# Kernel tuning notes

Measured on AMD Instinct MI355X. Metric: run time of the kernel, lower is better.

The kernel has to match this reference:

```python
import jax, jax.numpy as jnp
import numpy as np

ALPHA = 0.2  # LeakyReLU negative slope

def setup_inputs() -> dict:
    key = jax.random.key(0)
    k1, k2, k3 = jax.random.split(key, 3)
    N, F_in, F_out = 8192, 128, 64
    h = jax.random.normal(k1, (N, F_in), dtype=jnp.float32)
    W = jax.random.normal(k2, (F_in, F_out), dtype=jnp.float32) * 0.1
    a = jax.random.normal(k3, (2 * F_out, 1), dtype=jnp.float32) * 0.1
    return {"h": h, "W": W, "a": a}

def reference(h, W, a):
    # Wh: [N, F_out]
    Wh = h @ W
    F_out = Wh.shape[1]
    # Split 'a' into source/dest halves; e_ij = leakyrelu(a1.Wh_i + a2.Wh_j)
    a1 = a[:F_out, 0]   # [F_out]
    a2 = a[F_out:, 0]   # [F_out]
    e_src = Wh @ a1     # [N]
    e_dst = Wh @ a2     # [N]
    e = e_src[:, None] + e_dst[None, :]          # [N, N]
    e = jnp.where(e > 0, e, ALPHA * e)           # leaky relu
    attention = jax.nn.softmax(e, axis=1)        # dropout omitted (eval mode)
    h_prime = attention @ Wh                     # [N, F_out]
    return jax.nn.elu(h_prime)                   # concat=True path
```

## Files before the change

kernel.cpp:

```cpp
#include <hip/hip_runtime.h>


typedef unsigned long long ull;

constexpr int N_ROWS = 8192;
constexpr int F_IN   = 128;
constexpr int F_OUT  = 64;
#define LRELU_ALPHA 0.2f

constexpr int SBLK = 8;
constexpr int NGRP = N_ROWS / SBLK;

constexpr int WS_WH   = 0;
constexpr int WS_ESRC = WS_WH + N_ROWS * F_OUT;
constexpr int WS_KEYA = WS_ESRC + N_ROWS;
constexpr int WS_KEYB = WS_KEYA + 2 * N_ROWS;
constexpr int WS_GS1T = WS_KEYB + 2 * N_ROWS;
constexpr int WS_GS2T = WS_GS1T + F_OUT * NGRP;
constexpr int WS_GD1  = WS_GS2T + F_OUT * NGRP;
constexpr int WS_GD2  = WS_GD1 + NGRP;
constexpr int WS_P1   = WS_GD2 + NGRP;
constexpr int WS_P2   = WS_P1 + (NGRP + 1) * F_OUT;
constexpr int WS_D1   = WS_P2 + (NGRP + 1) * F_OUT;
constexpr int WS_D2   = WS_D1 + (NGRP + 1);
static_assert((WS_KEYA % 2) == 0 && (WS_KEYB % 2) == 0, "keys 8B-aligned");

__device__ __forceinline__ unsigned mono_enc(float f) {
  unsigned u = __float_as_uint(f);
  return u ^ ((u & 0x80000000u) ? 0xFFFFFFFFu : 0x80000000u);
}
__device__ __forceinline__ float mono_dec(unsigned e) {
  unsigned u = e ^ ((e & 0x80000000u) ? 0x80000000u : 0xFFFFFFFFu);
  return __uint_as_float(u);
}

__global__ __launch_bounds__(256) void k1_wh(const float* __restrict__ h,
                                             const float* __restrict__ W,
                                             const float* __restrict__ a,
                                             float* __restrict__ ws) {
  __shared__ float hlds[16 * F_IN];
  __shared__ float alds[2 * F_OUT];
  const int t = threadIdx.x;
  const int row0 = blockIdx.x * 16;

  const float4* hsrc = (const float4*)(h + (long)row0 * F_IN);
  float4* hd = (float4*)hlds;
  hd[t]       = hsrc[t];
  hd[t + 256] = hsrc[t + 256];
  if (t < 2 * F_OUT) alds[t] = a[t];
  __syncthreads();

  const int wave = t >> 6, lane = t & 63;
  const float* hp = hlds + (wave * 4) * F_IN;
  float acc0 = 0.f, acc1 = 0.f, acc2 = 0.f, acc3 = 0.f;

  #pragma unroll 4
  for (int k4 = 0; k4 < F_IN; k4 += 4) {
    float4 h0 = *(const float4*)(hp + k4);
    float4 h1 = *(const float4*)(hp + F_IN + k4);
    float4 h2 = *(const float4*)(hp + 2 * F_IN + k4);
    float4 h3 = *(const float4*)(hp + 3 * F_IN + k4);
    float w0 = W[(k4 + 0) * F_OUT + lane];
    float w1 = W[(k4 + 1) * F_OUT + lane];
    float w2 = W[(k4 + 2) * F_OUT + lane];
    float w3 = W[(k4 + 3) * F_OUT + lane];
    acc0 = fmaf(h0.x, w0, acc0); acc0 = fmaf(h0.y, w1, acc0);
    acc0 = fmaf(h0.z, w2, acc0); acc0 = fmaf(h0.w, w3, acc0);
    acc1 = fmaf(h1.x, w0, acc1); acc1 = fmaf(h1.y, w1, acc1);
    acc1 = fmaf(h1.z, w2, acc1); acc1 = fmaf(h1.w, w3, acc1);
    acc2 = fmaf(h2.x, w0, acc2); acc2 = fmaf(h2.y, w1, acc2);
    acc2 = fmaf(h2.z, w2, acc2); acc2 = fmaf(h2.w, w3, acc2);
    acc3 = fmaf(h3.x, w0, acc3); acc3 = fmaf(h3.y, w1, acc3);
    acc3 = fmaf(h3.z, w2, acc3); acc3 = fmaf(h3.w, w3, acc3);
  }

  const int grow = row0 + wave * 4;
  float* Wh = ws + WS_WH;
  Wh[(grow + 0) * F_OUT + lane] = acc0;
  Wh[(grow + 1) * F_OUT + lane] = acc1;
  Wh[(grow + 2) * F_OUT + lane] = acc2;
  Wh[(grow + 3) * F_OUT + lane] = acc3;

  const float a1 = alds[lane], a2 = alds[F_OUT + lane];
  float s0 = acc0 * a1, s1 = acc1 * a1, s2 = acc2 * a1, s3 = acc3 * a1;
  float d0 = acc0 * a2, d1 = acc1 * a2, d2 = acc2 * a2, d3 = acc3 * a2;
  #pragma unroll
  for (int off = 32; off; off >>= 1) {
    s0 += __shfl_down(s0, off); s1 += __shfl_down(s1, off);
    s2 += __shfl_down(s2, off); s3 += __shfl_down(s3, off);
    d0 += __shfl_down(d0, off); d1 += __shfl_down(d1, off);
    d2 += __shfl_down(d2, off); d3 += __shfl_down(d3, off);
  }
  if (lane == 0) {
    ws[WS_ESRC + grow + 0] = s0; ws[WS_ESRC + grow + 1] = s1;
    ws[WS_ESRC + grow + 2] = s2; ws[WS_ESRC + grow + 3] = s3;
    ull* keys = (ull*)(ws + WS_KEYA);
    keys[grow + 0] = ((ull)mono_enc(d0) << 32) | (unsigned)(grow + 0);
    keys[grow + 1] = ((ull)mono_enc(d1) << 32) | (unsigned)(grow + 1);
    keys[grow + 2] = ((ull)mono_enc(d2) << 32) | (unsigned)(grow + 2);
    keys[grow + 3] = ((ull)mono_enc(d3) << 32) | (unsigned)(grow + 3);
  }
}

__global__ __launch_bounds__(256) void k2a_local(ull* __restrict__ keys) {
  __shared__ ull lk[256];
  const int t = threadIdx.x;
  const int base = blockIdx.x * 256;
  lk[t] = keys[base + t];
  __syncthreads();
  for (int k = 2; k <= 256; k <<= 1) {
    for (int j = k >> 1; j > 0; j >>= 1) {
      int p = t ^ j;
      if (p > t) {
        ull x = lk[t], y = lk[p];
        bool asc = ((t & k) == 0);
        if ((x > y) == asc) { lk[t] = y; lk[p] = x; }
      }
      __syncthreads();
    }
  }
  keys[base + t] = lk[t];
}

template <int RUN>
__global__ __launch_bounds__(256) void k_merge(const ull* __restrict__ src,
                                               ull* __restrict__ dst) {
  const int g = blockIdx.x * 256 + threadIdx.x;
  const ull key = src[g];
  const int pairbase = g & ~(2 * RUN - 1);
  const int local = g - pairbase;
  const bool inA = local < RUN;
  const ull* other = src + pairbase + (inA ? RUN : 0);
  const int idx = inA ? local : (local - RUN);
  int lo = 0, hi = RUN;
  while (lo < hi) {
    int m = (lo + hi) >> 1;
    if (other[m] < key) lo = m + 1; else hi = m;
  }
  dst[pairbase + idx + lo] = key;
}

__global__ __launch_bounds__(256) void k3a_gs(float* __restrict__ ws) {
  const int t = threadIdx.x, wv = t >> 6, lane = t & 63;
  const int g = blockIdx.x * 4 + wv;
  const ull* K = (const ull*)(ws + WS_KEYB);
  const float* Wh = ws + WS_WH;
  float s1 = 0.f, s2 = 0.f, sd1 = 0.f, sd2 = 0.f;
  #pragma unroll
  for (int o = 0; o < SBLK; ++o) {
    ull key = K[(g << 3) + o];
    float d = mono_dec((unsigned)(key >> 32));
    int j = (int)(key & 0xFFFFFFFFu);
    float e1 = __expf(d), e2 = __expf(LRELU_ALPHA * d);
    float v = Wh[j * F_OUT + lane];
    s1 = fmaf(e1, v, s1); s2 = fmaf(e2, v, s2);
    sd1 += e1; sd2 += e2;
  }
  ws[WS_GS1T + lane * NGRP + g] = s1;
  ws[WS_GS2T + lane * NGRP + g] = s2;
  if (lane == 0) { ws[WS_GD1 + g] = sd1; ws[WS_GD2 + g] = sd2; }
}

__global__ __launch_bounds__(1024) void k3b_scan(float* __restrict__ ws) {
  __shared__ float sm[1024];
  const int t = threadIdx.x;
  const int blk = blockIdx.x;
  const float* src;
  int c = 0;
  if (blk < 64)        { c = blk;      src = ws + WS_GS1T + c * NGRP; }
  else if (blk < 128)  { c = blk - 64; src = ws + WS_GS2T + c * NGRP; }
  else if (blk == 128) { src = ws + WS_GD1; }
  else                 { src = ws + WS_GD2; }

  const float x = src[t];
  sm[t] = x;
  __syncthreads();
  for (int off = 1; off < 1024; off <<= 1) {
    float y = (t >= off) ? sm[t - off] : 0.f;
    __syncthreads();
    sm[t] += y;
    __syncthreads();
  }
  const float incl = sm[t];
  const float excl = incl - x;
  if (blk < 64) {
    ws[WS_P1 + t * F_OUT + c] = excl;
    if (t == NGRP - 1) ws[WS_P1 + NGRP * F_OUT + c] = incl;
  } else if (blk < 128) {
    ws[WS_P2 + t * F_OUT + c] = excl;
    if (t == NGRP - 1) ws[WS_P2 + NGRP * F_OUT + c] = incl;
  } else if (blk == 128) {
    ws[WS_D1 + t] = excl;
    if (t == NGRP - 1) ws[WS_D1 + NGRP] = incl;
  } else {
    ws[WS_D2 + t] = excl;
    if (t == NGRP - 1) ws[WS_D2 + NGRP] = incl;
  }
}

__global__ __launch_bounds__(256) void k4_out(const float* __restrict__ ws,
                                              float* __restrict__ out) {
  const int t = threadIdx.x, wv = t >> 6, lane = t & 63;
  const int i = blockIdx.x * 4 + wv;
  const ull* K = (const ull*)(ws + WS_KEYB);
  const float s = ws[WS_ESRC + i];
  const float ns = (s == 0.0f) ? 0.0f : -s;
  const unsigned Ki = mono_enc(ns);

  unsigned m1 = (unsigned)(K[lane << 7] >> 32);
  ull bal1 = __ballot(m1 <= Ki);
  int tl;
  if (bal1 == 0ull) {
    tl = 0;
  } else {
    int L1 = 63 - __clzll((long long)bal1);
    int base = L1 << 7;
    unsigned m2 = (unsigned)(K[base + (lane << 1)] >> 32);
    ull bal2 = __ballot(m2 <= Ki);
    int L2 = 63 - __clzll((long long)bal2);
    int p = base + (L2 << 1) + 1;
    unsigned m3 = (unsigned)(K[p] >> 32);
    tl = p + ((m3 <= Ki) ? 1 : 0);
  }
  const int b = tl >> 3, rr = tl & 7;

  float p1 = ws[WS_P1 + b * F_OUT + lane];
  float p2 = ws[WS_P2 + b * F_OUT + lane];
  float d1 = ws[WS_D1 + b], d2 = ws[WS_D2 + b];
  const float p1tot = ws[WS_P1 + NGRP * F_OUT + lane];
  const float d1tot = ws[WS_D1 + NGRP];
  const float* Wh = ws + WS_WH;

  for (int o = 0; o < rr; ++o) {
    ull key = K[(b << 3) + o];
    float d = mono_dec((unsigned)(key >> 32));
    int j = (int)(key & 0xFFFFFFFFu);
    float e1 = __expf(d), e2 = __expf(LRELU_ALPHA * d);
    float v = Wh[j * F_OUT + lane];
    p1 = fmaf(e1, v, p1); p2 = fmaf(e2, v, p2);
    d1 += e1; d2 += e2;
  }

  const float es1 = __expf(s), es2 = __expf(LRELU_ALPHA * s);
  const float num = es1 * (p1tot - p1) + es2 * p2;
  const float den = es1 * (d1tot - d1) + es2 * d2;
  const float r = num / den;
  out[i * F_OUT + lane] = (r > 0.f) ? r : (__expf(r) - 1.f);
}

extern "C" void kernel_launch(void* const* d_in, const int* in_sizes, int n_in,
                              void* d_out, int out_size, void* d_ws, size_t ws_size,
                              hipStream_t stream) {
  const float* h = (const float*)d_in[0];
  const float* W = (const float*)d_in[1];
  const float* a = (const float*)d_in[2];
  float* ws = (float*)d_ws;
  float* out = (float*)d_out;
  ull* keyA = (ull*)(ws + WS_KEYA);
  ull* keyB = (ull*)(ws + WS_KEYB);

  hipLaunchKernelGGL(k1_wh,         dim3(N_ROWS / 16), dim3(256),  0, stream, h, W, a, ws);
  hipLaunchKernelGGL(k2a_local,     dim3(32),          dim3(256),  0, stream, keyA);
  hipLaunchKernelGGL(k_merge<256>,  dim3(32),          dim3(256),  0, stream, keyA, keyB);
  hipLaunchKernelGGL(k_merge<512>,  dim3(32),          dim3(256),  0, stream, keyB, keyA);
  hipLaunchKernelGGL(k_merge<1024>, dim3(32),          dim3(256),  0, stream, keyA, keyB);
  hipLaunchKernelGGL(k_merge<2048>, dim3(32),          dim3(256),  0, stream, keyB, keyA);
  hipLaunchKernelGGL(k_merge<4096>, dim3(32),          dim3(256),  0, stream, keyA, keyB);
  hipLaunchKernelGGL(k3a_gs,        dim3(NGRP / 4),    dim3(256),  0, stream, ws);
  hipLaunchKernelGGL(k3b_scan,      dim3(130),         dim3(1024), 0, stream, ws);
  hipLaunchKernelGGL(k4_out,        dim3(N_ROWS / 4),  dim3(256),  0, stream, ws, out);
}
```

Baseline: 103.3 us.

## Replace merge cascade with single rank-based merge and fuse group-sum with scan

```diff
diff --git a/kernel.cpp b/kernel.cpp
--- a/kernel.cpp
+++ b/kernel.cpp
@@ -15,11 +15,7 @@
 constexpr int WS_ESRC = WS_WH + N_ROWS * F_OUT;
 constexpr int WS_KEYA = WS_ESRC + N_ROWS;
 constexpr int WS_KEYB = WS_KEYA + 2 * N_ROWS;
-constexpr int WS_GS1T = WS_KEYB + 2 * N_ROWS;
-constexpr int WS_GS2T = WS_GS1T + F_OUT * NGRP;
-constexpr int WS_GD1  = WS_GS2T + F_OUT * NGRP;
-constexpr int WS_GD2  = WS_GD1 + NGRP;
-constexpr int WS_P1   = WS_GD2 + NGRP;
+constexpr int WS_P1   = WS_KEYB + 2 * N_ROWS;
 constexpr int WS_P2   = WS_P1 + (NGRP + 1) * F_OUT;
 constexpr int WS_D1   = WS_P2 + (NGRP + 1) * F_OUT;
 constexpr int WS_D2   = WS_D1 + (NGRP + 1);
@@ -122,79 +118,87 @@
   keys[base + t] = lk[t];
 }
 
-template <int RUN>
-__global__ __launch_bounds__(256) void k_merge(const ull* __restrict__ src,
-                                               ull* __restrict__ dst) {
-  const int g = blockIdx.x * 256 + threadIdx.x;
-  const ull key = src[g];
-  const int pairbase = g & ~(2 * RUN - 1);
-  const int local = g - pairbase;
-  const bool inA = local < RUN;
-  const ull* other = src + pairbase + (inA ? RUN : 0);
-  const int idx = inA ? local : (local - RUN);
-  int lo = 0, hi = RUN;
-  while (lo < hi) {
-    int m = (lo + hi) >> 1;
-    if (other[m] < key) lo = m + 1; else hi = m;
-  }
-  dst[pairbase + idx + lo] = key;
-}
-
-__global__ __launch_bounds__(256) void k3a_gs(float* __restrict__ ws) {
-  const int t = threadIdx.x, wv = t >> 6, lane = t & 63;
-  const int g = blockIdx.x * 4 + wv;
-  const ull* K = (const ull*)(ws + WS_KEYB);
+__global__ __launch_bounds__(256) void k_merge32(const ull* __restrict__ keyA,
+                                                 ull* __restrict__ keyB) {
+  const int gt = blockIdx.x * 256 + threadIdx.x;
+  const int elem = gt >> 3, sub = gt & 7;
+  const ull key = keyA[elem];
+  const int r0 = elem >> 8;
+  int cnt = 0;
+  #pragma unroll
+  for (int rr = 0; rr < 4; ++rr) {
+    const int r = sub * 4 + rr;
+    if (r == r0) continue;
+    const ull* run = keyA + (r << 8);
+    if (run[255] < key) {
+      cnt += 256;
+    } else {
+      int lo = 0;
+      #pragma unroll
+      for (int step = 128; step; step >>= 1)
+        lo += (run[lo + step - 1] < key) ? step : 0;
+      cnt += lo;
+    }
+  }
+  cnt += __shfl_down(cnt, 4);
+  cnt += __shfl_down(cnt, 2);
+  cnt += __shfl_down(cnt, 1);
+  if (sub == 0) keyB[cnt + (elem & 255)] = key;
+}
+
+__global__ __launch_bounds__(256) void k3_tables(float* __restrict__ ws) {
+  __shared__ float2 sm[256];
+  const ull* keyB = (const ull*)(ws + WS_KEYB);
   const float* Wh = ws + WS_WH;
-  float s1 = 0.f, s2 = 0.f, sd1 = 0.f, sd2 = 0.f;
-  #pragma unroll
-  for (int o = 0; o < SBLK; ++o) {
-    ull key = K[(g << 3) + o];
-    float d = mono_dec((unsigned)(key >> 32));
-    int j = (int)(key & 0xFFFFFFFFu);
-    float e1 = __expf(d), e2 = __expf(LRELU_ALPHA * d);
-    float v = Wh[j * F_OUT + lane];
-    s1 = fmaf(e1, v, s1); s2 = fmaf(e2, v, s2);
-    sd1 += e1; sd2 += e2;
-  }
-  ws[WS_GS1T + lane * NGRP + g] = s1;
-  ws[WS_GS2T + lane * NGRP + g] = s2;
-  if (lane == 0) { ws[WS_GD1 + g] = sd1; ws[WS_GD2 + g] = sd2; }
-}
-
-__global__ __launch_bounds__(1024) void k3b_scan(float* __restrict__ ws) {
-  __shared__ float sm[1024];
   const int t = threadIdx.x;
-  const int blk = blockIdx.x;
-  const float* src;
-  int c = 0;
-  if (blk < 64)        { c = blk;      src = ws + WS_GS1T + c * NGRP; }
-  else if (blk < 128)  { c = blk - 64; src = ws + WS_GS2T + c * NGRP; }
-  else if (blk == 128) { src = ws + WS_GD1; }
-  else                 { src = ws + WS_GD2; }
-
-  const float x = src[t];
-  sm[t] = x;
+  const int c = blockIdx.x;
+  const bool isD = (c == F_OUT);
+
+  float g1[4], g2[4];
+  for (int gg = 0; gg < 4; ++gg) {
+    const int g = t * 4 + gg;
+    float s1 = 0.f, s2 = 0.f;
+    #pragma unroll
+    for (int o = 0; o < SBLK; ++o) {
+      ull key = keyB[(g << 3) + o];
+      float d = mono_dec((unsigned)(key >> 32));
+      int j = (int)(key & 0xFFFFFFFFu) & (N_ROWS - 1);
+      float e1 = __expf(d), e2 = __expf(LRELU_ALPHA * d);
+      float v = isD ? 1.0f : Wh[j * F_OUT + c];
+      s1 = fmaf(e1, v, s1); s2 = fmaf(e2, v, s2);
+    }
+    g1[gg] = s1; g2[gg] = s2;
+  }
+  const float tot1 = g1[0] + g1[1] + g1[2] + g1[3];
+  const float tot2 = g2[0] + g2[1] + g2[2] + g2[3];
+  sm[t] = make_float2(tot1, tot2);
   __syncthreads();
-  for (int off = 1; off < 1024; off <<= 1) {
-    float y = (t >= off) ? sm[t - off] : 0.f;
+  for (int off = 1; off < 256; off <<= 1) {
+    float2 y = (t >= off) ? sm[t - off] : make_float2(0.f, 0.f);
     __syncthreads();
-    sm[t] += y;
+    sm[t].x += y.x; sm[t].y += y.y;
     __syncthreads();
   }
-  const float incl = sm[t];
-  const float excl = incl - x;
-  if (blk < 64) {
-    ws[WS_P1 + t * F_OUT + c] = excl;
-    if (t == NGRP - 1) ws[WS_P1 + NGRP * F_OUT + c] = incl;
-  } else if (blk < 128) {
-    ws[WS_P2 + t * F_OUT + c] = excl;
-    if (t == NGRP - 1) ws[WS_P2 + NGRP * F_OUT + c] = incl;
-  } else if (blk == 128) {
-    ws[WS_D1 + t] = excl;
-    if (t == NGRP - 1) ws[WS_D1 + NGRP] = incl;
-  } else {
-    ws[WS_D2 + t] = excl;
-    if (t == NGRP - 1) ws[WS_D2 + NGRP] = incl;
+  float p1 = sm[t].x - tot1, p2 = sm[t].y - tot2;
+  for (int gg = 0; gg < 4; ++gg) {
+    const int g = t * 4 + gg;
+    if (!isD) {
+      ws[WS_P1 + g * F_OUT + c] = p1;
+      ws[WS_P2 + g * F_OUT + c] = p2;
+    } else {
+      ws[WS_D1 + g] = p1;
+      ws[WS_D2 + g] = p2;
+    }
+    p1 += g1[gg]; p2 += g2[gg];
+  }
+  if (t == 255) {
+    if (!isD) {
+      ws[WS_P1 + NGRP * F_OUT + c] = p1;
+      ws[WS_P2 + NGRP * F_OUT + c] = p2;
+    } else {
+      ws[WS_D1 + NGRP] = p1;
+      ws[WS_D2 + NGRP] = p2;
+    }
   }
 }
 
@@ -234,7 +238,7 @@
   for (int o = 0; o < rr; ++o) {
     ull key = K[(b << 3) + o];
     float d = mono_dec((unsigned)(key >> 32));
-    int j = (int)(key & 0xFFFFFFFFu);
+    int j = (int)(key & 0xFFFFFFFFu) & (N_ROWS - 1);
     float e1 = __expf(d), e2 = __expf(LRELU_ALPHA * d);
     float v = Wh[j * F_OUT + lane];
     p1 = fmaf(e1, v, p1); p2 = fmaf(e2, v, p2);
@@ -259,14 +263,9 @@
   ull* keyA = (ull*)(ws + WS_KEYA);
   ull* keyB = (ull*)(ws + WS_KEYB);
 
-  hipLaunchKernelGGL(k1_wh,         dim3(N_ROWS / 16), dim3(256),  0, stream, h, W, a, ws);
-  hipLaunchKernelGGL(k2a_local,     dim3(32),          dim3(256),  0, stream, keyA);
-  hipLaunchKernelGGL(k_merge<256>,  dim3(32),          dim3(256),  0, stream, keyA, keyB);
-  hipLaunchKernelGGL(k_merge<512>,  dim3(32),          dim3(256),  0, stream, keyB, keyA);
-  hipLaunchKernelGGL(k_merge<1024>, dim3(32),          dim3(256),  0, stream, keyA, keyB);
-  hipLaunchKernelGGL(k_merge<2048>, dim3(32),          dim3(256),  0, stream, keyB, keyA);
-  hipLaunchKernelGGL(k_merge<4096>, dim3(32),          dim3(256),  0, stream, keyA, keyB);
-  hipLaunchKernelGGL(k3a_gs,        dim3(NGRP / 4),    dim3(256),  0, stream, ws);
-  hipLaunchKernelGGL(k3b_scan,      dim3(130),         dim3(1024), 0, stream, ws);
-  hipLaunchKernelGGL(k4_out,        dim3(N_ROWS / 4),  dim3(256),  0, stream, ws, out);
-}
+  hipLaunchKernelGGL(k1_wh,     dim3(N_ROWS / 16), dim3(256), 0, stream, h, W, a, ws);
+  hipLaunchKernelGGL(k2a_local, dim3(32),          dim3(256), 0, stream, keyA);
+  hipLaunchKernelGGL(k_merge32, dim3(256),         dim3(256), 0, stream, keyA, keyB);
+  hipLaunchKernelGGL(k3_tables, dim3(F_OUT + 1),   dim3(256), 0, stream, ws);
+  hipLaunchKernelGGL(k4_out,    dim3(N_ROWS / 4),  dim3(256), 0, stream, ws, out);
+}
```

Measured after the change: 105.4 us. No clear change (+2.0%).
